# Optimization experiments

Hardware: AMD Instinct MI355X
Metric: run time of the kernel (lower is better)

The kernel has to match this reference:

```python
import jax, jax.numpy as jnp
import numpy as np

D_MODEL = 2048
N_HEADS = 16
D_K = D_MODEL // N_HEADS
D_FF = 5504
THETA = 10000.0
EPS = 1e-5


def rmsnorm(x, g):
    xf = x.astype(jnp.float32)
    ms = jnp.mean(xf * xf, axis=-1, keepdims=True)
    return (xf / jnp.sqrt(ms + EPS) * g).astype(x.dtype)


def rope_tables(seq_len):
    k = jnp.arange(D_K // 2, dtype=jnp.float32)
    freqs = THETA ** (-2.0 * k / float(D_K))          # [d_k/2]
    pos = jnp.arange(seq_len, dtype=jnp.float32)
    phases = pos[:, None] * freqs[None, :]            # [S, d_k/2]
    return jnp.cos(phases), jnp.sin(phases)


def apply_rope(x, cos, sin):
    # x: [..., S, d_k]; cos/sin: [S, d_k/2]
    x_even = x[..., 0::2]
    x_odd = x[..., 1::2]
    e = x_even * cos - x_odd * sin
    o = x_even * sin + x_odd * cos
    out = jnp.stack([e, o], axis=-1)                  # [..., S, d_k/2, 2]
    return out.reshape(x.shape)


def setup_inputs() -> dict:
    key = jax.random.key(0)
    ks = jax.random.split(key, 9)
    def tn(k, shape, fan_in, fan_out):
        std = np.sqrt(2.0 / (fan_in + fan_out))
        return (jax.random.truncated_normal(k, -3.0, 3.0, shape, jnp.float32) * std)
    B, S = 2, 2048
    return {
        "x": jax.random.normal(ks[0], (B, S, D_MODEL), jnp.float32),
        "Wq": tn(ks[1], (D_MODEL, D_MODEL), D_MODEL, D_MODEL),
        "Wk": tn(ks[2], (D_MODEL, D_MODEL), D_MODEL, D_MODEL),
        "Wv": tn(ks[3], (D_MODEL, D_MODEL), D_MODEL, D_MODEL),
        "Wo": tn(ks[4], (D_MODEL, D_MODEL), D_MODEL, D_MODEL),
        "W1": tn(ks[5], (D_FF, D_MODEL), D_MODEL, D_FF),
        "W2": tn(ks[6], (D_MODEL, D_FF), D_FF, D_MODEL),
        "W3": tn(ks[7], (D_FF, D_MODEL), D_MODEL, D_FF),
        "g1": jnp.ones((D_MODEL,), jnp.float32),
        "g2": jnp.ones((D_MODEL,), jnp.float32),
    }


def reference(x, Wq, Wk, Wv, Wo, W1, W2, W3, g1, g2):
    B, S, D = x.shape
    # --- attention sublayer (pre-norm) ---
    xn = rmsnorm(x, g1)
    q = jnp.einsum('bsd,ed->bse', xn, Wq).reshape(B, S, N_HEADS, D_K).transpose(0, 2, 1, 3)
    k = jnp.einsum('bsd,ed->bse', xn, Wk).reshape(B, S, N_HEADS, D_K).transpose(0, 2, 1, 3)
    v = jnp.einsum('bsd,ed->bse', xn, Wv).reshape(B, S, N_HEADS, D_K).transpose(0, 2, 1, 3)
    cos, sin = rope_tables(S)
    q = apply_rope(q, cos, sin)
    k = apply_rope(k, cos, sin)
    scores = jnp.einsum('bhqd,bhkd->bhqk', q, k) / jnp.sqrt(jnp.float32(D_K))
    causal = jnp.tril(jnp.ones((S, S), bool))         # True = keep
    scores = jnp.where(causal, scores, -jnp.inf)
    attn = jax.nn.softmax(scores, axis=-1)
    out = jnp.einsum('bhqk,bhkd->bhqd', attn, v)
    out = out.transpose(0, 2, 1, 3).reshape(B, S, D)
    out = jnp.einsum('bse,de->bsd', out, Wo)
    x_res = x + out
    # --- SwiGLU FFN sublayer (pre-norm) ---
    xn2 = rmsnorm(x_res, g2)
    w1x = jnp.einsum('bsd,fd->bsf', xn2, W1)
    w3x = jnp.einsum('bsd,fd->bsf', xn2, W3)
    h = (w1x * jax.nn.sigmoid(w1x)) * w3x
    ff = jnp.einsum('bsf,df->bsd', h, W2)
    return x_res + ff
```

## Files before the change

kernel.cpp:

```cpp
#include <hip/hip_runtime.h>
#include <hip/hip_bf16.h>
#include <math.h>


typedef __bf16 bf16x8 __attribute__((ext_vector_type(8)));
typedef float f32x4 __attribute__((ext_vector_type(4)));

#define MFMA16(a, b, c) __builtin_amdgcn_mfma_f32_16x16x32_bf16(a, b, c, 0, 0, 0)

__device__ __forceinline__ void async_cp16(const void* g, void* l) {
  __builtin_amdgcn_global_load_lds((__attribute__((address_space(1))) void*)g,
                                   (__attribute__((address_space(3))) void*)l,
                                   16, 0, 0);
}

__global__ __launch_bounds__(256) void cvt_k(const float* __restrict__ s,
                                             __bf16* __restrict__ d, long n) {
  const long i = ((long)blockIdx.x * 256 + threadIdx.x) * 8;
  if (i >= n) return;
  f32x4 a = *(const f32x4*)(s + i);
  f32x4 b = *(const f32x4*)(s + i + 4);
  bf16x8 o;
#pragma unroll
  for (int j = 0; j < 4; ++j) {
    o[j] = (__bf16)a[j];
    o[4 + j] = (__bf16)b[j];
  }
  *(bf16x8*)(d + i) = o;
}

template <int EPI, typename CT, typename RT>
__global__ __launch_bounds__(256) void gemm_bt(
    const __bf16* __restrict__ A, const __bf16* __restrict__ B,
    CT* C, const RT* R, int M, int N, int K) {
  __shared__ __attribute__((aligned(16))) __bf16 sA[128 * 32];
  __shared__ __attribute__((aligned(16))) __bf16 sB[128 * 32];
  const int tid = threadIdx.x;
  const int lane = tid & 63;
  const int wave = tid >> 6;
  const int wm = (wave >> 1) << 6;
  const int wn = (wave & 1) << 6;
  const int ln15 = lane & 15;
  const int kq8 = (lane >> 4) << 3;
  const long blockM = (long)blockIdx.y << 7;
  const long blockN = (long)blockIdx.x << 7;

  const int srow = tid >> 2;
  const int scol = (tid & 3) << 3;
  const __bf16* gA = A + (blockM + srow) * (long)K + scol;
  const __bf16* gB = B + (blockN + srow) * (long)K + scol;
  __bf16* lA = sA + tid * 8;
  __bf16* lB = sB + tid * 8;

  f32x4 acc[4][4] = {};
  const int KT = K >> 5;

  async_cp16(gA, lA);
  async_cp16(gA + 64 * (long)K, lA + 2048);
  async_cp16(gB, lB);
  async_cp16(gB + 64 * (long)K, lB + 2048);

  for (int kt = 0; kt < KT; ++kt) {
    __builtin_amdgcn_s_waitcnt(0);
    __syncthreads();
    bf16x8 af[4], bfr[4];
#pragma unroll
    for (int i = 0; i < 4; ++i)
      af[i] = *(const bf16x8*)&sA[(wm + i * 16 + ln15) * 32 + kq8];
#pragma unroll
    for (int j = 0; j < 4; ++j)
      bfr[j] = *(const bf16x8*)&sB[(wn + j * 16 + ln15) * 32 + kq8];
    __syncthreads();
    if (kt + 1 < KT) {
      const __bf16* a2 = gA + (long)(kt + 1) * 32;
      const __bf16* b2 = gB + (long)(kt + 1) * 32;
      async_cp16(a2, lA);
      async_cp16(a2 + 64 * (long)K, lA + 2048);
      async_cp16(b2, lB);
      async_cp16(b2 + 64 * (long)K, lB + 2048);
    }
#pragma unroll
    for (int i = 0; i < 4; ++i)
#pragma unroll
      for (int j = 0; j < 4; ++j)
        acc[i][j] = MFMA16(af[i], bfr[j], acc[i][j]);
  }

  const int rq4 = (lane >> 4) << 2;
#pragma unroll
  for (int i = 0; i < 4; ++i)
#pragma unroll
    for (int j = 0; j < 4; ++j)
#pragma unroll
      for (int r = 0; r < 4; ++r) {
        const long grow = blockM + wm + i * 16 + rq4 + r;
        const long gcol = blockN + wn + j * 16 + ln15;
        const long idx = grow * N + gcol;
        float v = acc[i][j][r];
        if (EPI == 1) v += (float)R[idx];
        if (EPI == 2) {
          const float w = (float)R[idx];
          v *= w / (1.f + __expf(-w));
        }
        C[idx] = (CT)v;
      }
}

__device__ __forceinline__ void sm_update(const f32x4 s[2], float mrow[4],
                                          float lrow[4], f32x4 oacc[8],
                                          __bf16* sP, int qb, int kbase,
                                          int ln15, int quad) {
  const float scale = 0.08838834764831845f;
  const float NEG = -1.0e4f;
#pragma unroll
  for (int r = 0; r < 4; ++r) {
    const int qrow = qb + quad * 4 + r;
    const bool m0 = (kbase + ln15 > qrow);
    const bool m1 = (kbase + 16 + ln15 > qrow);
    const float s0 = m0 ? NEG : s[0][r] * scale;
    const float s1 = m1 ? NEG : s[1][r] * scale;
    float tm = fmaxf(s0, s1);
#pragma unroll
    for (int off = 1; off < 16; off <<= 1) tm = fmaxf(tm, __shfl_xor(tm, off));
    const float mnew = fmaxf(mrow[r], tm);
    const float alpha = __expf(mrow[r] - mnew);
    mrow[r] = mnew;
    const float p0 = m0 ? 0.f : __expf(s0 - mnew);
    const float p1 = m1 ? 0.f : __expf(s1 - mnew);
    float rs = p0 + p1;
#pragma unroll
    for (int off = 1; off < 16; off <<= 1) rs += __shfl_xor(rs, off);
    lrow[r] = lrow[r] * alpha + rs;
#pragma unroll
    for (int nt = 0; nt < 8; ++nt) oacc[nt][r] *= alpha;
    sP[(quad * 4 + r) * 32 + ln15] = (__bf16)p0;
    sP[(quad * 4 + r) * 32 + 16 + ln15] = (__bf16)p1;
  }
}

__global__ __launch_bounds__(64, 2) void attn_k(
    const __bf16* __restrict__ q, const __bf16* __restrict__ k,
    const __bf16* __restrict__ v, __bf16* __restrict__ o) {
  __shared__ __attribute__((aligned(16))) __bf16 sPA[16 * 32];
  __shared__ __attribute__((aligned(16))) __bf16 sPB[16 * 32];
  const int lane = threadIdx.x;
  const int ln15 = lane & 15;
  const int quad = lane >> 4;
  const int lin = blockIdx.x + 64 * (blockIdx.y + 16 * blockIdx.z);
  const int xcd = lin & 7;
  const int j = lin >> 3;
  const int panel = xcd * 4 + (j >> 6);
  const int p = j & 63;
  const int b = panel >> 4;
  const int h = panel & 15;
  const int S = 2048;
  const int qbA = p << 4;
  const int qbB = (127 - p) << 4;
  const long bh = (long)b * S * 2048 + h * 128;

  bf16x8 qfA[4], qfB[4];
  {
    const __bf16* qpA = q + bh + (long)(qbA + ln15) * 2048 + quad * 8;
    const __bf16* qpB = q + bh + (long)(qbB + ln15) * 2048 + quad * 8;
#pragma unroll
    for (int kb = 0; kb < 4; ++kb) {
      qfA[kb] = *(const bf16x8*)(qpA + kb * 32);
      qfB[kb] = *(const bf16x8*)(qpB + kb * 32);
    }
  }

  const float NEG = -1.0e4f;
  f32x4 oaccA[8] = {}, oaccB[8] = {};
  float mrowA[4] = {NEG, NEG, NEG, NEG}, mrowB[4] = {NEG, NEG, NEG, NEG};
  float lrowA[4] = {}, lrowB[4] = {};

  const int nktA = ((p) + 2) >> 1;
  const int nktB = ((127 - p) + 2) >> 1;

  for (int kt = 0; kt < nktB; ++kt) {
    const int kbase = kt << 5;
    const bool doA = (kt < nktA);
    f32x4 sA[2] = {}, sB[2] = {};
    if (doA) {
#pragma unroll
      for (int c = 0; c < 2; ++c) {
        const __bf16* kp =
            k + bh + (long)(kbase + c * 16 + ln15) * 2048 + quad * 8;
#pragma unroll
        for (int kb = 0; kb < 4; ++kb) {
          bf16x8 kf = *(const bf16x8*)(kp + kb * 32);
          sB[c] = MFMA16(qfB[kb], kf, sB[c]);
          sA[c] = MFMA16(qfA[kb], kf, sA[c]);
        }
      }
    } else {
#pragma unroll
      for (int c = 0; c < 2; ++c) {
        const __bf16* kp =
            k + bh + (long)(kbase + c * 16 + ln15) * 2048 + quad * 8;
#pragma unroll
        for (int kb = 0; kb < 4; ++kb) {
          bf16x8 kf = *(const bf16x8*)(kp + kb * 32);
          sB[c] = MFMA16(qfB[kb], kf, sB[c]);
        }
      }
    }

    sm_update(sB, mrowB, lrowB, oaccB, sPB, qbB, kbase, ln15, quad);
    if (doA) sm_update(sA, mrowA, lrowA, oaccA, sPA, qbA, kbase, ln15, quad);

    __syncthreads();
    bf16x8 paB = *(const bf16x8*)&sPB[ln15 * 32 + quad * 8];
    bf16x8 paA = {};
    if (doA) paA = *(const bf16x8*)&sPA[ln15 * 32 + quad * 8];
    __syncthreads();

    const __bf16* vbase = v + bh + (long)kbase * 2048;
    if (doA) {
#pragma unroll
      for (int nt = 0; nt < 8; ++nt) {
        bf16x8 vf;
        const __bf16* vp = vbase + (long)(quad * 8) * 2048 + nt * 16 + ln15;
#pragma unroll
        for (int jj = 0; jj < 8; ++jj) vf[jj] = vp[(long)jj * 2048];
        oaccB[nt] = MFMA16(paB, vf, oaccB[nt]);
        oaccA[nt] = MFMA16(paA, vf, oaccA[nt]);
      }
    } else {
#pragma unroll
      for (int nt = 0; nt < 8; ++nt) {
        bf16x8 vf;
        const __bf16* vp = vbase + (long)(quad * 8) * 2048 + nt * 16 + ln15;
#pragma unroll
        for (int jj = 0; jj < 8; ++jj) vf[jj] = vp[(long)jj * 2048];
        oaccB[nt] = MFMA16(paB, vf, oaccB[nt]);
      }
    }
  }

  __bf16* opB = o + bh + (long)qbB * 2048;
  __bf16* opA = o + bh + (long)qbA * 2048;
#pragma unroll
  for (int nt = 0; nt < 8; ++nt)
#pragma unroll
    for (int r = 0; r < 4; ++r) {
      opB[(long)(quad * 4 + r) * 2048 + nt * 16 + ln15] =
          (__bf16)(oaccB[nt][r] / lrowB[r]);
      opA[(long)(quad * 4 + r) * 2048 + nt * 16 + ln15] =
          (__bf16)(oaccA[nt][r] / lrowA[r]);
    }
}

__global__ __launch_bounds__(256) void rmsnorm_k(
    const float* __restrict__ x, const float* __restrict__ g,
    __bf16* __restrict__ out) {
  __shared__ float red[4];
  const int row = blockIdx.x;
  const int tid = threadIdx.x;
  f32x4 xa = *(const f32x4*)(x + (long)row * 2048 + tid * 8);
  f32x4 xb = *(const f32x4*)(x + (long)row * 2048 + tid * 8 + 4);
  float xf[8];
  float ss = 0.f;
#pragma unroll
  for (int j = 0; j < 4; ++j) {
    xf[j] = xa[j];
    xf[4 + j] = xb[j];
  }
#pragma unroll
  for (int j = 0; j < 8; ++j) ss += xf[j] * xf[j];
#pragma unroll
  for (int off = 32; off > 0; off >>= 1) ss += __shfl_xor(ss, off);
  if ((tid & 63) == 0) red[tid >> 6] = ss;
  __syncthreads();
  const float inv = rsqrtf((red[0] + red[1] + red[2] + red[3]) * (1.f / 2048.f) + 1e-5f);
  f32x4 ga = *(const f32x4*)(g + tid * 8);
  f32x4 gb = *(const f32x4*)(g + tid * 8 + 4);
  bf16x8 ov;
#pragma unroll
  for (int j = 0; j < 4; ++j) {
    ov[j] = (__bf16)(xf[j] * inv * ga[j]);
    ov[4 + j] = (__bf16)(xf[4 + j] * inv * gb[j]);
  }
  *(bf16x8*)(out + (long)row * 2048 + tid * 8) = ov;
}

__global__ __launch_bounds__(256) void rope_k(__bf16* __restrict__ t) {
  const long idx = (long)blockIdx.x * 256 + threadIdx.x;
  const int kp = idx & 63;
  const int h = (idx >> 6) & 15;
  const long row = idx >> 10;
  const int pos = (int)(row & 2047);
  const float freq = exp2f((float)kp * (-13.287712379549449f / 64.0f));
  float sn, cs;
  sincosf((float)pos * freq, &sn, &cs);
  __bf16* p = t + row * 2048 + h * 128 + kp * 2;
  const float e = (float)p[0], od = (float)p[1];
  p[0] = (__bf16)(e * cs - od * sn);
  p[1] = (__bf16)(e * sn + od * cs);
}

extern "C" void kernel_launch(void* const* d_in, const int* in_sizes, int n_in,
                              void* d_out, int out_size, void* d_ws, size_t ws_size,
                              hipStream_t stream) {
  const float* x = (const float*)d_in[0];
  const float* Wq = (const float*)d_in[1];
  const float* Wk = (const float*)d_in[2];
  const float* Wv = (const float*)d_in[3];
  const float* Wo = (const float*)d_in[4];
  const float* W1 = (const float*)d_in[5];
  const float* W2 = (const float*)d_in[6];
  const float* W3 = (const float*)d_in[7];
  const float* g1 = (const float*)d_in[8];
  const float* g2 = (const float*)d_in[9];
  float* out = (float*)d_out;
  char* ws = (char*)d_ws;

  const long NDD = 2048L * 2048;
  const long NFD = 5504L * 2048;
  const long WSLOT = 22544384;
  const long MB16 = 16777216;

  __bf16* wslot = (__bf16*)(ws);
  __bf16* xn = (__bf16*)(ws + WSLOT);
  __bf16* qb = (__bf16*)(ws + WSLOT + MB16);
  __bf16* kb = (__bf16*)(ws + WSLOT + 2 * MB16);
  __bf16* vb = (__bf16*)(ws + WSLOT + 3 * MB16);
  __bf16* attn = xn;
  __bf16* xn2 = vb;
  __bf16* w1x = xn;

  rmsnorm_k<<<4096, 256, 0, stream>>>(x, g1, xn);

  cvt_k<<<2048, 256, 0, stream>>>(Wq, wslot, NDD);
  gemm_bt<0, __bf16, float><<<dim3(16, 32), 256, 0, stream>>>(
      xn, wslot, qb, nullptr, 4096, 2048, 2048);
  cvt_k<<<2048, 256, 0, stream>>>(Wk, wslot, NDD);
  gemm_bt<0, __bf16, float><<<dim3(16, 32), 256, 0, stream>>>(
      xn, wslot, kb, nullptr, 4096, 2048, 2048);
  cvt_k<<<2048, 256, 0, stream>>>(Wv, wslot, NDD);
  gemm_bt<0, __bf16, float><<<dim3(16, 32), 256, 0, stream>>>(
      xn, wslot, vb, nullptr, 4096, 2048, 2048);

  rope_k<<<16384, 256, 0, stream>>>(qb);
  rope_k<<<16384, 256, 0, stream>>>(kb);
  attn_k<<<dim3(64, 16, 2), 64, 0, stream>>>(qb, kb, vb, attn);

  cvt_k<<<2048, 256, 0, stream>>>(Wo, wslot, NDD);
  gemm_bt<1, float, float><<<dim3(16, 32), 256, 0, stream>>>(
      attn, wslot, out, x, 4096, 2048, 2048);

  rmsnorm_k<<<4096, 256, 0, stream>>>(out, g2, xn2);

  cvt_k<<<5504, 256, 0, stream>>>(W1, wslot, NFD);
  gemm_bt<0, __bf16, float><<<dim3(43, 32), 256, 0, stream>>>(
      xn2, wslot, w1x, nullptr, 4096, 5504, 2048);
  cvt_k<<<5504, 256, 0, stream>>>(W3, wslot, NFD);
  gemm_bt<2, __bf16, __bf16><<<dim3(43, 32), 256, 0, stream>>>(
      xn2, wslot, w1x, w1x, 4096, 5504, 2048);
  cvt_k<<<5504, 256, 0, stream>>>(W2, wslot, NFD);
  gemm_bt<1, float, float><<<dim3(16, 32), 256, 0, stream>>>(
      w1x, wslot, out, out, 4096, 2048, 5504);
}
```

Measured before the change: 1.028 ms.

## Double GEMM K-tile to 64 with XOR-swizzled LDS layout

```diff
diff --git a/kernel.cpp b/kernel.cpp
--- a/kernel.cpp
+++ b/kernel.cpp
@@ -33,57 +33,70 @@
 __global__ __launch_bounds__(256) void gemm_bt(
     const __bf16* __restrict__ A, const __bf16* __restrict__ B,
     CT* C, const RT* R, int M, int N, int K) {
-  __shared__ __attribute__((aligned(16))) __bf16 sA[128 * 32];
-  __shared__ __attribute__((aligned(16))) __bf16 sB[128 * 32];
+  __shared__ __attribute__((aligned(16))) __bf16 sA[128 * 64];
+  __shared__ __attribute__((aligned(16))) __bf16 sB[128 * 64];
   const int tid = threadIdx.x;
   const int lane = tid & 63;
   const int wave = tid >> 6;
   const int wm = (wave >> 1) << 6;
   const int wn = (wave & 1) << 6;
   const int ln15 = lane & 15;
-  const int kq8 = (lane >> 4) << 3;
+  const int quad = lane >> 4;
   const long blockM = (long)blockIdx.y << 7;
   const long blockN = (long)blockIdx.x << 7;
 
-  const int srow = tid >> 2;
-  const int scol = (tid & 3) << 3;
-  const __bf16* gA = A + (blockM + srow) * (long)K + scol;
-  const __bf16* gB = B + (blockN + srow) * (long)K + scol;
+  const int srow = tid >> 3;
+  const int scolb = ((tid & 7) ^ (srow & 7)) << 4;
+  const __bf16* gA = A + (blockM + srow) * (long)K + (scolb >> 1);
+  const __bf16* gB = B + (blockN + srow) * (long)K + (scolb >> 1);
   __bf16* lA = sA + tid * 8;
   __bf16* lB = sB + tid * 8;
 
   f32x4 acc[4][4] = {};
-  const int KT = K >> 5;
-
-  async_cp16(gA, lA);
-  async_cp16(gA + 64 * (long)K, lA + 2048);
-  async_cp16(gB, lB);
-  async_cp16(gB + 64 * (long)K, lB + 2048);
+  const int KT = K >> 6;
+
+#pragma unroll
+  for (int rr = 0; rr < 4; ++rr) {
+    async_cp16(gA + (long)rr * 32 * K, lA + rr * 2048);
+    async_cp16(gB + (long)rr * 32 * K, lB + rr * 2048);
+  }
+
+  const char* sAb = (const char*)sA;
+  const char* sBb = (const char*)sB;
+  const int rsw = (ln15 & 7) << 4;
+  const int cbk[2] = {(quad << 4) ^ rsw, (64 | (quad << 4)) ^ rsw};
 
   for (int kt = 0; kt < KT; ++kt) {
     __builtin_amdgcn_s_waitcnt(0);
     __syncthreads();
-    bf16x8 af[4], bfr[4];
-#pragma unroll
-    for (int i = 0; i < 4; ++i)
-      af[i] = *(const bf16x8*)&sA[(wm + i * 16 + ln15) * 32 + kq8];
-#pragma unroll
-    for (int j = 0; j < 4; ++j)
-      bfr[j] = *(const bf16x8*)&sB[(wn + j * 16 + ln15) * 32 + kq8];
+    bf16x8 af[2][4], bfr[2][4];
+#pragma unroll
+    for (int i = 0; i < 4; ++i) {
+      const int ra = (wm + i * 16 + ln15) << 7;
+      const int rb = (wn + i * 16 + ln15) << 7;
+#pragma unroll
+      for (int kk = 0; kk < 2; ++kk) {
+        af[kk][i] = *(const bf16x8*)(sAb + ra + cbk[kk]);
+        bfr[kk][i] = *(const bf16x8*)(sBb + rb + cbk[kk]);
+      }
+    }
     __syncthreads();
     if (kt + 1 < KT) {
-      const __bf16* a2 = gA + (long)(kt + 1) * 32;
-      const __bf16* b2 = gB + (long)(kt + 1) * 32;
-      async_cp16(a2, lA);
-      async_cp16(a2 + 64 * (long)K, lA + 2048);
-      async_cp16(b2, lB);
-      async_cp16(b2 + 64 * (long)K, lB + 2048);
-    }
-#pragma unroll
-    for (int i = 0; i < 4; ++i)
-#pragma unroll
-      for (int j = 0; j < 4; ++j)
-        acc[i][j] = MFMA16(af[i], bfr[j], acc[i][j]);
+      const __bf16* a2 = gA + (long)(kt + 1) * 64;
+      const __bf16* b2 = gB + (long)(kt + 1) * 64;
+#pragma unroll
+      for (int rr = 0; rr < 4; ++rr) {
+        async_cp16(a2 + (long)rr * 32 * K, lA + rr * 2048);
+        async_cp16(b2 + (long)rr * 32 * K, lB + rr * 2048);
+      }
+    }
+#pragma unroll
+    for (int kk = 0; kk < 2; ++kk)
+#pragma unroll
+      for (int i = 0; i < 4; ++i)
+#pragma unroll
+        for (int j = 0; j < 4; ++j)
+          acc[i][j] = MFMA16(af[kk][i], bfr[kk][j], acc[i][j]);
   }
 
   const int rq4 = (lane >> 4) << 2;
```

Result: faster. 1.001 ms (-2.6%).
